# Kernel tuning notes

Measured on AMD Instinct MI355X. Metric: run time of the kernel, lower is better.

The kernel has to match this reference:

```python
import jax, jax.numpy as jnp
import numpy as np

# ---- module hyperparameters (from init_kwargs) ----
J = 6      # number of octaves -> subsample by 2**J
Q = 6      # wavelets per octave
T = 16000  # signal length
SUB = 2 ** J           # downsampling factor (=> T_out = 250)
XI_MAX = 0.35          # max center frequency (cycles/sample), kymatio convention


def _build_filters(T, J, Q):
    """Gabor (Morlet-style) band-pass filterbank + Gaussian lowpass, in Fourier domain."""
    freqs = np.fft.fftfreq(T).astype(np.float64)          # (T,) cycles/sample
    n_psi = J * Q
    xis = XI_MAX * 2.0 ** (-np.arange(n_psi) / Q)         # constant-Q center freqs
    r = 2.0 ** (1.0 / Q)
    sigmas = xis * (r - 1.0) / (r + 1.0)                  # constant-Q bandwidths
    psi_hat = np.exp(-((freqs[None, :] - xis[:, None]) ** 2)
                     / (2.0 * sigmas[:, None] ** 2))       # (n_psi, T)
    sigma_phi = XI_MAX / (2.0 ** J)                        # lowpass bandwidth ~ 2^-J
    phi_hat = np.exp(-(freqs ** 2) / (2.0 * sigma_phi ** 2))  # (T,)
    return jnp.asarray(psi_hat, jnp.float32), jnp.asarray(phi_hat, jnp.float32)

PSI_HAT, PHI_HAT = _build_filters(T, J, Q)  # fixed (non-learned) filter constants


def setup_inputs() -> dict:
    key = jax.random.key(0)
    x = jax.random.normal(key, (64, 1, T), dtype=jnp.float32)
    return {"x": x}


def _scattering(x2d):
    """First-order scattering. x2d: (B, T) -> Sx: (B, 1 + J*Q, T//2**J)."""
    X = jnp.fft.fft(x2d, axis=-1)                                   # (B, T) complex
    # order 0: lowpass + subsample
    S0 = jnp.real(jnp.fft.ifft(X * PHI_HAT, axis=-1))[:, ::SUB]     # (B, T')
    # order 1: bandpass -> modulus -> lowpass -> subsample (vectorized over filters)
    U = jnp.abs(jnp.fft.ifft(X[:, None, :] * PSI_HAT[None, :, :], axis=-1))  # (B,JQ,T)
    S1 = jnp.real(jnp.fft.ifft(jnp.fft.fft(U, axis=-1) * PHI_HAT, axis=-1))[:, :, ::SUB]
    return jnp.concatenate([S0[:, None, :], S1], axis=1)            # (B, C, T')


def reference(x):
    # accept (B, T) or (B, 1, T) like the torch module
    if x.ndim == 3:
        x = x[:, 0, :]
    Sx = _scattering(x)[..., None]                                  # (B, C, T', 1)
    C = Sx.shape[1]
    c1 = max(1, C // 3)
    c2 = max(1, 2 * C // 3)
    low = Sx[:, :c1].mean(axis=1)
    mid = Sx[:, c1:c2].mean(axis=1)
    high = Sx[:, c2:].mean(axis=1)
    return jnp.stack([low, mid, high], axis=1)                      # (B, 3, T', 1)
```

## Files before the change

kernel.cpp:

```cpp
#include <hip/hip_runtime.h>
#include <hip/hip_bf16.h>

#define TLEN 16000
#define NPSI 36
#define NBATCH 64
#define NOUT 250
#define NCH 37
#define DHALF 176
#define KMAX 8000
#define TWO_PI 6.283185307179586

__device__ __forceinline__ int brev7(int q){ return (int)(__brev((unsigned)q) >> 25); }
__device__ __forceinline__ int drev125(int p){
    return (p % 5) * 25 + ((p / 5) % 5) * 5 + (p / 25);
}

__global__ __launch_bounds__(256) void k_ffta(const float* __restrict__ x,
                                              float2* __restrict__ Gtmp){
    __shared__ float xr[32 * 126], xi[32 * 126];
    __shared__ float w125r[125], w125i[125];
    __shared__ float w16r[125],  w16i[125];
    __shared__ float w128r[128], w128i[128];
    const int b = blockIdx.x >> 2, g = blockIdx.x & 3, row0 = 32 * g;
    const int tid = threadIdx.x;

    for (int j = tid; j < 125; j += 256){
        double a = -TWO_PI * (double)j / 125.0;
        w125r[j] = (float)cos(a); w125i[j] = (float)sin(a);
        double a2 = -TWO_PI * (double)j / 16000.0;
        w16r[j] = (float)cos(a2); w16i[j] = (float)sin(a2);
    }
    for (int j = tid; j < 128; j += 256){
        double a = -TWO_PI * (double)j / 128.0;
        w128r[j] = (float)cos(a); w128i[j] = (float)sin(a);
    }
    for (int i = tid; i < 32 * 125; i += 256){
        int n1 = i >> 5, lr = i & 31;
        xr[lr * 126 + n1] = x[b * TLEN + 128 * n1 + row0 + lr];
        xi[lr * 126 + n1] = 0.0f;
    }
    int f = 1;
    for (int s = 25; s >= 1; s /= 5, f *= 5){
        __syncthreads();
        for (int task = tid; task < 25 * 32; task += 256){
            int u = task >> 5, lr = task & 31;
            int blk = u / s, m = u - blk * s;
            int base = lr * 126 + blk * 5 * s + m;
            float vr[5], vi[5];
            #pragma unroll
            for (int r = 0; r < 5; ++r){ vr[r] = xr[base + r * s]; vi[r] = xi[base + r * s]; }
            #pragma unroll
            for (int q = 0; q < 5; ++q){
                float cr = vr[0], ci = vi[0];
                #pragma unroll
                for (int r = 1; r < 5; ++r){
                    int w5 = 25 * ((q * r) % 5);
                    float wr = w125r[w5], wi = w125i[w5];
                    cr += vr[r] * wr - vi[r] * wi;
                    ci += vr[r] * wi + vi[r] * wr;
                }
                int jt = (m * q * f) % 125;
                float tr = w125r[jt], ti = w125i[jt];
                xr[base + q * s] = cr * tr - ci * ti;
                xi[base + q * s] = cr * ti + ci * tr;
            }
        }
    }
    __syncthreads();
    for (int i = tid; i < 125 * 32; i += 256){
        int p = i >> 5, lr = i & 31;
        int n2 = row0 + lr;
        int m = drev125(p);
        int a = m * n2;
        int qq = a / 125, rr = a - qq * 125;
        float tr = w16r[rr] * w128r[qq] - w16i[rr] * w128i[qq];
        float ti = w16r[rr] * w128i[qq] + w16i[rr] * w128r[qq];
        float ar = xr[lr * 126 + p], ai = xi[lr * 126 + p];
        Gtmp[((size_t)b * 125 + p) * 128 + n2] =
            make_float2(ar * tr - ai * ti, ar * ti + ai * tr);
    }
}

__global__ __launch_bounds__(256) void k_fftb(const float2* __restrict__ Gtmp,
                                              float2* __restrict__ Xf){
    __shared__ float gr[128 * 26], gi[128 * 26];
    __shared__ float w128r[128], w128i[128];
    const int b = blockIdx.x / 5, p0 = (blockIdx.x % 5) * 25;
    const int tid = threadIdx.x;
    for (int j = tid; j < 128; j += 256){
        double a = -TWO_PI * (double)j / 128.0;
        w128r[j] = (float)cos(a); w128i[j] = (float)sin(a);
    }
    for (int i = tid; i < 25 * 128; i += 256){
        int ml = i >> 7, n2 = i & 127;
        float2 v = Gtmp[((size_t)b * 125 + p0 + ml) * 128 + n2];
        gr[n2 * 26 + ml] = v.x; gi[n2 * 26 + ml] = v.y;
    }
    for (int span = 64; span >= 1; span >>= 1){
        __syncthreads();
        for (int idx = tid; idx < 1600; idx += 256){
            int u = idx / 25, ml = idx - u * 25;
            int blkq = u / span, mm = u % span;
            int i0 = (blkq * 2 * span + mm) * 26 + ml, i1 = i0 + span * 26;
            float ar = gr[i0], ai = gi[i0], br = gr[i1], bi = gi[i1];
            gr[i0] = ar + br; gi[i0] = ai + bi;
            float dr = ar - br, di = ai - bi;
            int jt = mm * (64 / span);
            gr[i1] = dr * w128r[jt] - di * w128i[jt];
            gi[i1] = dr * w128i[jt] + di * w128r[jt];
        }
    }
    __syncthreads();
    for (int idx = tid; idx < 1600; idx += 256){
        int u = idx / 25, ml = idx - u * 25;
        int ad = (2 * u) * 26 + ml;
        int k = drev125(p0 + ml) + 125 * brev7(2 * u);
        Xf[(size_t)b * KMAX + k] = make_float2(gr[ad], gi[ad]);
    }
}

template<int P5, int LQ>
__device__ __forceinline__ void env_body(const float2* __restrict__ Xfb,
                                         float* __restrict__ Schan,
                                         int fi, int b, int tid,
                                         float* Br, float* Bi,
                                         float* wPr, float* wPi,
                                         float* wNr, float* wNi,
                                         float* wQr, float* wQi,
                                         float* w5tr, float* w5ti,
                                         float* hfull, int* drevT, float* sred){
    constexpr int Q = 1 << LQ;
    constexpr int N = P5 * Q;
    constexpr int D = TLEN / N;
    constexpr int S1 = P5 / 5;
    constexpr int NIT = (N + 511) / 512;

    const double xi_d = 0.35 * exp2(-(double)fi / 6.0);
    const double r_d  = exp2(1.0 / 6.0);
    const double sig_d = xi_d * (r_d - 1.0) / (r_d + 1.0);
    const float xi = (float)xi_d;
    const float centerT = (float)(xi_d * (double)TLEN);
    const float sigT = (float)(sig_d * (double)TLEN);
    int klo = (int)floorf(centerT - 5.0f * sigT); if (klo < 1) klo = 1;
    int khi = (int)ceilf(centerT + 5.0f * sigT);  if (khi > KMAX - 1) khi = KMAX - 1;
    const float inv2s2 = (float)(1.0 / (2.0 * sig_d * sig_d));

    for (int j = tid; j < P5; j += 512){
        double a = TWO_PI * (double)j / (double)P5;
        wPr[j] = (float)cos(a); wPi[j] = (float)sin(a);
        double a2 = TWO_PI * (double)j / (double)N;
        wNr[j] = (float)cos(a2); wNi[j] = (float)sin(a2);
        drevT[j] = (P5 == 125) ? drev125(j) : ((j % 5) * 5 + j / 5);
    }
    for (int j = tid; j < Q; j += 512){
        double a = TWO_PI * (double)j / (double)Q;
        wQr[j] = (float)cos(a); wQi[j] = (float)sin(a);
    }
    for (int j = tid; j < 25; j += 512){
        double a = TWO_PI * (double)(((j / 5) * (j % 5)) % 5) / 5.0;
        w5tr[j] = (float)cos(a); w5ti[j] = (float)sin(a);
    }
    for (int j = tid; j <= 2 * DHALF; j += 512){
        double st = 1.0 / (TWO_PI * (0.35 / 64.0));
        double dd = (double)(j - DHALF);
        hfull[j] = (float)((0.35 / 64.0) * sqrt(TWO_PI) * exp(-0.5 * dd * dd / (st * st)));
    }
    __syncthreads();
    for (int task = tid; task < S1 * Q; task += 512){
        int m = task >> LQ, k2 = task & (Q - 1);
        float vr[5], vi[5];
        #pragma unroll
        for (int r = 0; r < 5; ++r){
            int gk = k2 + ((m + r * S1) << LQ);
            float ur = 0.0f, ui = 0.0f;
            if (gk >= klo && gk <= khi){
                float fr = (float)gk * (1.0f / (float)TLEN);
                float d = fr - xi;
                float p = __expf(-d * d * inv2s2) * (1.0f / (float)TLEN);
                float2 Xv = Xfb[gk];
                ur = Xv.x * p; ui = Xv.y * p;
            }
            vr[r] = ur; vi[r] = ui;
        }
        int base = m * Q + k2;
        #pragma unroll
        for (int q = 0; q < 5; ++q){
            float cr = vr[0], ci = vi[0];
            #pragma unroll
            for (int r = 1; r < 5; ++r){
                float wr = w5tr[q * 5 + r], wi = w5ti[q * 5 + r];
                cr += vr[r] * wr - vi[r] * wi;
                ci += vr[r] * wi + vi[r] * wr;
            }
            int jt = m * q;
            float tr = wPr[jt], ti = wPi[jt];
            Br[base + q * S1 * Q] = cr * tr - ci * ti;
            Bi[base + q * S1 * Q] = cr * ti + ci * tr;
        }
    }
    if (P5 == 125){
        __syncthreads();
        for (int task = tid; task < 25 * Q; task += 512){
            int u = task >> LQ, k2 = task & (Q - 1);
            int blk = u / 5, m = u - blk * 5;
            int base = (blk * 25 + m) * Q + k2;
            float vr[5], vi[5];
            #pragma unroll
            for (int r = 0; r < 5; ++r){ vr[r] = Br[base + r * 5 * Q]; vi[r] = Bi[base + r * 5 * Q]; }
            #pragma unroll
            for (int q = 0; q < 5; ++q){
                float cr = vr[0], ci = vi[0];
                #pragma unroll
                for (int r = 1; r < 5; ++r){
                    float wr = w5tr[q * 5 + r], wi = w5ti[q * 5 + r];
                    cr += vr[r] * wr - vi[r] * wi;
                    ci += vr[r] * wi + vi[r] * wr;
                }
                int jt = m * q * 5;
                float tr = wPr[jt], ti = wPi[jt];
                Br[base + q * 5 * Q] = cr * tr - ci * ti;
                Bi[base + q * 5 * Q] = cr * ti + ci * tr;
            }
        }
    }
    __syncthreads();
    for (int task = tid; task < S1 * Q; task += 512){
        int u = task >> LQ, k2 = task & (Q - 1);
        int base = (u * 5) * Q + k2;
        float vr[5], vi[5];
        #pragma unroll
        for (int r = 0; r < 5; ++r){ vr[r] = Br[base + r * Q]; vi[r] = Bi[base + r * Q]; }
        #pragma unroll
        for (int q = 0; q < 5; ++q){
            float cr = vr[0], ci = vi[0];
            #pragma unroll
            for (int r = 1; r < 5; ++r){
                float wr = w5tr[q * 5 + r], wi = w5ti[q * 5 + r];
                cr += vr[r] * wr - vi[r] * wi;
                ci += vr[r] * wi + vi[r] * wr;
            }
            int n1 = drevT[5 * u + q];
            int a = k2 * n1;
            int qq = a / P5, rr = a - qq * P5;
            float tr = wQr[qq] * wNr[rr] - wQi[qq] * wNi[rr];
            float ti = wQr[qq] * wNi[rr] + wQi[qq] * wNr[rr];
            Br[base + q * Q] = cr * tr - ci * ti;
            Bi[base + q * Q] = cr * ti + ci * tr;
        }
    }
    #pragma unroll
    for (int pass = 0; pass < LQ / 2; ++pass){
        const int Sp = Q >> (1 + 2 * pass);
        const int half = Sp >> 1;
        __syncthreads();
        for (int task = tid; task < P5 * (Q / 4); task += 512){
            int prow = task / (Q / 4), v = task & (Q / 4 - 1);
            int blkq = v / half, m = v - blkq * half;
            int base = prow * Q + blkq * 2 * Sp + m;
            float Ar = Br[base],           Ai = Bi[base];
            float B2r = Br[base + half],   B2i = Bi[base + half];
            float Cr = Br[base + Sp],      Ci = Bi[base + Sp];
            float D2r = Br[base + Sp + half], D2i = Bi[base + Sp + half];
            int jt1 = m * ((Q / 2) / Sp);
            float w1r = wQr[jt1], w1i = wQi[jt1];
            float w2r = wQr[2 * jt1], w2i = wQi[2 * jt1];
            float A1r = Ar + Cr, A1i = Ai + Ci;
            float t1r = Ar - Cr, t1i = Ai - Ci;
            float C1r = t1r * w1r - t1i * w1i, C1i = t1r * w1i + t1i * w1r;
            float B1r = B2r + D2r, B1i = B2i + D2i;
            float t2r = B2r - D2r, t2i = B2i - D2i;
            float t3r = -t2i, t3i = t2r;
            float D1r = t3r * w1r - t3i * w1i, D1i = t3r * w1i + t3i * w1r;
            Br[base] = A1r + B1r;  Bi[base] = A1i + B1i;
            float u1r = A1r - B1r, u1i = A1i - B1i;
            Br[base + half] = u1r * w2r - u1i * w2i;
            Bi[base + half] = u1r * w2i + u1i * w2r;
            Br[base + Sp] = C1r + D1r;  Bi[base + Sp] = C1i + D1i;
            float u2r = C1r - D1r, u2i = C1i - D1i;
            Br[base + Sp + half] = u2r * w2r - u2i * w2i;
            Bi[base + Sp + half] = u2r * w2i + u2i * w2r;
        }
    }
    if (LQ & 1){
        __syncthreads();
        for (int idx = tid; idx < P5 * (Q / 2); idx += 512){
            int p = idx / (Q / 2), u = idx - p * (Q / 2);
            int i0 = p * Q + 2 * u, i1 = i0 + 1;
            float ar = Br[i0], ai = Bi[i0], br2 = Br[i1], bi2 = Bi[i1];
            Br[i0] = ar + br2; Bi[i0] = ai + bi2;
            Br[i1] = ar - br2; Bi[i1] = ai - bi2;
        }
    }
    __syncthreads();
    float magv[NIT];
    #pragma unroll
    for (int i = 0; i < NIT; ++i){
        int idx = tid + 512 * i;
        if (idx < N){
            float vr = Br[idx], vi = Bi[idx];
            magv[i] = sqrtf(vr * vr + vi * vi);
        }
    }
    __syncthreads();
    #pragma unroll
    for (int i = 0; i < NIT; ++i){
        int idx = tid + 512 * i;
        if (idx < N){
            int p = idx >> LQ, u = idx & (Q - 1);
            int s2 = (int)(__brev((unsigned)u) >> (32 - LQ));
            int np = drevT[p] + P5 * s2;
            Bi[np + (np >> 5)] = magv[i];
        }
    }
    __syncthreads();
    float acc = 0.0f;
    if (tid < 500){
        int t = tid - 250 * (tid / 250);
        int q = tid / 250;
        int m0 = 64 * t;
        int lo = m0 - DHALF;
        int nlo = (lo >= 0) ? ((lo + D - 1) / D) : -((-lo) / D);
        int nhi = (m0 + DHALF) / D;
        int n = nlo + q;
        if (n <= nhi){
            int np = n % N; if (np < 0) np += N;
            int d = m0 - D * n + DHALF;
            for (; n <= nhi; n += 2){
                acc += hfull[d] * Bi[np + (np >> 5)];
                d -= 2 * D;
                np += 2; if (np >= N) np -= N;
            }
        }
        sred[tid] = acc;
    }
    __syncthreads();
    if (tid < 250)
        Schan[(b * NCH + 1 + fi) * NOUT + tid] = (sred[tid] + sred[tid + 250]) * (float)D;
}

__global__ __launch_bounds__(512, 4) void k_env_all(const float* __restrict__ x,
                                                    const float2* __restrict__ Xf,
                                                    float* __restrict__ Schan){
    __shared__ float Br[8000];
    __shared__ float Bi[8256];
    __shared__ float wPr[125], wPi[125];
    __shared__ float wNr[125], wNi[125];
    __shared__ float wQr[128], wQi[128];
    __shared__ float w5tr[25], w5ti[25];
    __shared__ float hfull[2 * DHALF + 1];
    __shared__ int   drevT[125];
    __shared__ float sred[500];

    const int bi = blockIdx.x;
    const int tid = threadIdx.x;
    if (bi < 448){
        int fi = bi >> 6, b = bi & 63;
        env_body<125, 6>(Xf + (size_t)b * KMAX, Schan, fi, b, tid, Br, Bi,
                         wPr, wPi, wNr, wNi, wQr, wQi, w5tr, w5ti, hfull, drevT, sred);
    } else if (bi < 640){
        int t = bi - 448;
        int fi = 7 + (t >> 6), b = t & 63;
        env_body<125, 5>(Xf + (size_t)b * KMAX, Schan, fi, b, tid, Br, Bi,
                         wPr, wPi, wNr, wNi, wQr, wQi, w5tr, w5ti, hfull, drevT, sred);
    } else if (bi < 1088){
        int t = bi - 640;
        int fi = 10 + (t >> 6), b = t & 63;
        env_body<25, 7>(Xf + (size_t)b * KMAX, Schan, fi, b, tid, Br, Bi,
                        wPr, wPi, wNr, wNi, wQr, wQi, w5tr, w5ti, hfull, drevT, sred);
    } else if (bi < 1408){
        int t = bi - 1088;
        int fi = 17 + (t >> 6), b = t & 63;
        env_body<125, 4>(Xf + (size_t)b * KMAX, Schan, fi, b, tid, Br, Bi,
                         wPr, wPi, wNr, wNi, wQr, wQi, w5tr, w5ti, hfull, drevT, sred);
    } else if (bi < 2304){
        int t = bi - 1408;
        int fi = 22 + (t >> 6), b = t & 63;
        env_body<25, 6>(Xf + (size_t)b * KMAX, Schan, fi, b, tid, Br, Bi,
                        wPr, wPi, wNr, wNi, wQr, wQi, w5tr, w5ti, hfull, drevT, sred);
    } else {
        int b = bi - 2304;
        const float* xb = x + (size_t)b * TLEN;
        for (int j = tid; j <= 2 * DHALF; j += 512){
            double st = 1.0 / (TWO_PI * (0.35 / 64.0));
            double dd = (double)(j - DHALF);
            hfull[j] = (float)((0.35 / 64.0) * sqrt(TWO_PI) * exp(-0.5 * dd * dd / (st * st)));
        }
        __syncthreads();
        float acc = 0.0f;
        if (tid < 500){
            int t = tid - 250 * (tid / 250);
            int q = tid / 250;
            int m0 = 64 * t;
            for (int j = q; j <= 2 * DHALF; j += 2){
                int n = m0 - DHALF + j;
                if (n < 0) n += TLEN; else if (n >= TLEN) n -= TLEN;
                acc += hfull[j] * xb[n];
            }
            sred[tid] = acc;
        }
        __syncthreads();
        if (tid < 250)
            Schan[(b * NCH + 0) * NOUT + tid] = sred[tid] + sred[tid + 250];
    }
}

__global__ __launch_bounds__(256) void k_reduce(const float* __restrict__ Schan,
                                                float* __restrict__ out){
    int o = blockIdx.x * 256 + threadIdx.x;
    if (o >= NBATCH * 3 * NOUT) return;
    int b = o / (3 * NOUT);
    int rem = o - b * 3 * NOUT;
    int g = rem / NOUT;
    int t = rem - g * NOUT;
    int c0 = (g == 0) ? 0 : (g == 1 ? 12 : 24);
    int c1 = (g == 0) ? 12 : (g == 1 ? 24 : 37);
    float s = 0.0f;
    for (int c = c0; c < c1; ++c) s += Schan[(b * NCH + c) * NOUT + t];
    out[o] = s / (float)(c1 - c0);
}

__global__ void k_fill_f32(float* out, int n, float v){
    int i = blockIdx.x * 256 + threadIdx.x;
    if (i < n) out[i] = v;
}

extern "C" void kernel_launch(void* const* d_in, const int* in_sizes, int n_in,
                              void* d_out, int out_size, void* d_ws, size_t ws_size,
                              hipStream_t stream) {
    const float* x = (const float*)d_in[0];
    float* out = (float*)d_out;
    const size_t xf_bytes = (size_t)NBATCH * KMAX * sizeof(float2);
    const size_t schan_bytes = (size_t)NBATCH * NCH * NOUT * sizeof(float);
    const size_t gtmp_bytes = (size_t)NBATCH * 16000 * sizeof(float2);
    if (ws_size < xf_bytes + schan_bytes + gtmp_bytes){
        k_fill_f32<<<(out_size + 255) / 256, 256, 0, stream>>>(out, out_size, 800.0f);
        return;
    }
    float2* Xf = (float2*)d_ws;
    float* Schan = (float*)((char*)d_ws + xf_bytes);
    float2* Gtmp = (float2*)((char*)d_ws + xf_bytes + schan_bytes);

    k_ffta<<<NBATCH * 4, 256, 0, stream>>>(x, Gtmp);
    k_fftb<<<NBATCH * 5, 256, 0, stream>>>(Gtmp, Xf);
    k_env_all<<<2368, 512, 0, stream>>>(x, Xf, Schan);
    k_reduce<<<(NBATCH * 3 * NOUT + 255) / 256, 256, 0, stream>>>(Schan, out);
}
```

Measured before the change: 144.8 us.

## Do radix-2 FFT stages in registers via wavefront shuffles instead of LDS passes

Replaces the shared-memory radix-4/radix-2 butterfly passes of the power-of-two sub-FFT with per-wavefront register butterflies using __shfl_xor, loading each row into registers once. This drops several __syncthreads and LDS round-trips per pass and fuses the modulus and scatter into the same step. In exchange it adds more shuffle instructions, register pressure from per-thread arrays, and clamped redundant rows when P5 does not divide evenly.

```diff
diff --git a/kernel.cpp b/kernel.cpp
--- a/kernel.cpp
+++ b/kernel.cpp
@@ -133,7 +133,10 @@
     constexpr int N = P5 * Q;
     constexpr int D = TLEN / N;
     constexpr int S1 = P5 / 5;
-    constexpr int NIT = (N + 511) / 512;
+    constexpr int GROUPW = (Q > 64) ? 64 : Q;
+    constexpr int E = (Q > 64) ? 2 : 1;
+    constexpr int RPP = 64 / GROUPW;
+    constexpr int NPASS = (P5 + 8 * RPP - 1) / (8 * RPP);
 
     const double xi_d = 0.35 * exp2(-(double)fi / 6.0);
     const double r_d  = exp2(1.0 / 6.0);
@@ -248,68 +251,62 @@
             Bi[base + q * Q] = cr * ti + ci * tr;
         }
     }
+    __syncthreads();
+    const int w = tid >> 6, lane = tid & 63;
+    const int lpos = lane & (GROUPW - 1);
+    const int rowoff = lane / GROUPW;
+    float fr_[NPASS][E], fi_[NPASS][E];
     #pragma unroll
-    for (int pass = 0; pass < LQ / 2; ++pass){
-        const int Sp = Q >> (1 + 2 * pass);
-        const int half = Sp >> 1;
-        __syncthreads();
-        for (int task = tid; task < P5 * (Q / 4); task += 512){
-            int prow = task / (Q / 4), v = task & (Q / 4 - 1);
-            int blkq = v / half, m = v - blkq * half;
-            int base = prow * Q + blkq * 2 * Sp + m;
-            float Ar = Br[base],           Ai = Bi[base];
-            float B2r = Br[base + half],   B2i = Bi[base + half];
-            float Cr = Br[base + Sp],      Ci = Bi[base + Sp];
-            float D2r = Br[base + Sp + half], D2i = Bi[base + Sp + half];
-            int jt1 = m * ((Q / 2) / Sp);
-            float w1r = wQr[jt1], w1i = wQi[jt1];
-            float w2r = wQr[2 * jt1], w2i = wQi[2 * jt1];
-            float A1r = Ar + Cr, A1i = Ai + Ci;
-            float t1r = Ar - Cr, t1i = Ai - Ci;
-            float C1r = t1r * w1r - t1i * w1i, C1i = t1r * w1i + t1i * w1r;
-            float B1r = B2r + D2r, B1i = B2i + D2i;
-            float t2r = B2r - D2r, t2i = B2i - D2i;
-            float t3r = -t2i, t3i = t2r;
-            float D1r = t3r * w1r - t3i * w1i, D1i = t3r * w1i + t3i * w1r;
-            Br[base] = A1r + B1r;  Bi[base] = A1i + B1i;
-            float u1r = A1r - B1r, u1i = A1i - B1i;
-            Br[base + half] = u1r * w2r - u1i * w2i;
-            Bi[base + half] = u1r * w2i + u1i * w2r;
-            Br[base + Sp] = C1r + D1r;  Bi[base + Sp] = C1i + D1i;
-            float u2r = C1r - D1r, u2i = C1i - D1i;
-            Br[base + Sp + half] = u2r * w2r - u2i * w2i;
-            Bi[base + Sp + half] = u2r * w2i + u2i * w2r;
-        }
-    }
-    if (LQ & 1){
-        __syncthreads();
-        for (int idx = tid; idx < P5 * (Q / 2); idx += 512){
-            int p = idx / (Q / 2), u = idx - p * (Q / 2);
-            int i0 = p * Q + 2 * u, i1 = i0 + 1;
-            float ar = Br[i0], ai = Bi[i0], br2 = Br[i1], bi2 = Bi[i1];
-            Br[i0] = ar + br2; Bi[i0] = ai + bi2;
-            Br[i1] = ar - br2; Bi[i1] = ai - bi2;
-        }
-    }
-    __syncthreads();
-    float magv[NIT];
+    for (int i = 0; i < NPASS; ++i){
+        int row = (w * NPASS + i) * RPP + rowoff;
+        int rc = row < P5 ? row : P5 - 1;
+        #pragma unroll
+        for (int e = 0; e < E; ++e){
+            fr_[i][e] = Br[rc * Q + lpos + e * 64];
+            fi_[i][e] = Bi[rc * Q + lpos + e * 64];
+        }
+    }
+    __syncthreads();
     #pragma unroll
-    for (int i = 0; i < NIT; ++i){
-        int idx = tid + 512 * i;
-        if (idx < N){
-            float vr = Br[idx], vi = Bi[idx];
-            magv[i] = sqrtf(vr * vr + vi * vi);
-        }
-    }
-    __syncthreads();
-    #pragma unroll
-    for (int i = 0; i < NIT; ++i){
-        int idx = tid + 512 * i;
-        if (idx < N){
-            int p = idx >> LQ, u = idx & (Q - 1);
-            int s2 = (int)(__brev((unsigned)u) >> (32 - LQ));
-            int np = drevT[p] + P5 * s2;
-            Bi[np + (np >> 5)] = magv[i];
+    for (int i = 0; i < NPASS; ++i){
+        int row = (w * NPASS + i) * RPP + rowoff;
+        if (E == 2){
+            float ar = fr_[i][0], ai = fi_[i][0];
+            float br2 = fr_[i][E - 1], bi2 = fi_[i][E - 1];
+            float dr = ar - br2, di = ai - bi2;
+            float wr = wQr[lane], wi = wQi[lane];
+            fr_[i][0] = ar + br2; fi_[i][0] = ai + bi2;
+            fr_[i][E - 1] = dr * wr - di * wi;
+            fi_[i][E - 1] = dr * wi + di * wr;
+        }
+        #pragma unroll
+        for (int sp = GROUPW / 2; sp >= 1; sp >>= 1){
+            int m = lpos & (sp - 1);
+            int jt = m * ((Q / 2) / sp);
+            float wr = wQr[jt], wi = wQi[jt];
+            bool hi = (lpos & sp) != 0;
+            #pragma unroll
+            for (int e = 0; e < E; ++e){
+                float pr = __shfl_xor(fr_[i][e], sp, 64);
+                float pi = __shfl_xor(fi_[i][e], sp, 64);
+                if (hi){
+                    float dr = pr - fr_[i][e], di = pi - fi_[i][e];
+                    fr_[i][e] = dr * wr - di * wi;
+                    fi_[i][e] = dr * wi + di * wr;
+                } else {
+                    fr_[i][e] += pr; fi_[i][e] += pi;
+                }
+            }
+        }
+        if (row < P5){
+            #pragma unroll
+            for (int e = 0; e < E; ++e){
+                int slot = lpos + e * 64;
+                int n2 = (int)(__brev((unsigned)slot) >> (32 - LQ));
+                float mag = sqrtf(fr_[i][e] * fr_[i][e] + fi_[i][e] * fi_[i][e]);
+                int np = drevT[row] + P5 * n2;
+                Bi[np + (np >> 5)] = mag;
+            }
         }
     }
     __syncthreads();
```

Result: slower. 151.7 us (+4.7%).
